# Kernel tuning notes

Measured on AMD Instinct MI355X. Metric: run time of the kernel, lower is better.

## Reference

```python
import jax, jax.numpy as jnp
import numpy as np

N_NODES = 50000
N_EDGES = 600000  # incidence entries; hyperedge ids also live in [0, N_NODES)
HID = 128


def _prelu(x, a):
    return jnp.where(x >= 0, x, a * x)


def _hypergraph_conv(x, W, b, node_idx, edge_idx, num_nodes, num_hedges):
    # PyG HypergraphConv (use_attention=False, heads=1):
    # out = D^{-1} H B^{-1} H^T (X Theta) + bias
    xw = x @ W  # [N, F]
    ones = jnp.ones(node_idx.shape[0], dtype=x.dtype)
    D = jax.ops.segment_sum(ones, node_idx, num_segments=num_nodes)   # node degree
    B = jax.ops.segment_sum(ones, edge_idx, num_segments=num_hedges)  # hyperedge degree
    Dinv = jnp.where(D > 0, 1.0 / D, 0.0)
    Binv = jnp.where(B > 0, 1.0 / B, 0.0)
    # node -> hyperedge aggregation, scaled by B^{-1}
    m = jax.ops.segment_sum(xw[node_idx], edge_idx, num_segments=num_hedges) * Binv[:, None]
    # hyperedge -> node aggregation, scaled by D^{-1}
    out = jax.ops.segment_sum(m[edge_idx], node_idx, num_segments=num_nodes) * Dinv[:, None]
    return out + b


def setup_inputs() -> dict:
    key = jax.random.key(0)
    k1, k2, k3, k4, k5 = jax.random.split(key, 5)
    x = jax.random.normal(k1, (N_NODES, HID), dtype=jnp.float32)
    hyper_edge_index = jax.random.randint(k2, (2, N_EDGES), 0, N_NODES, dtype=jnp.int64)
    # kaiming-normal-ish linear weights, zero biases (per init_weights)
    std = float(np.sqrt(2.0 / HID))
    W1 = jax.random.normal(k3, (HID, HID), dtype=jnp.float32) * std
    W2 = jax.random.normal(k4, (HID, HID), dtype=jnp.float32) * std
    b1 = jnp.zeros((HID,), dtype=jnp.float32)
    b2 = jnp.zeros((HID,), dtype=jnp.float32)
    prelu_a = jnp.full((1,), 0.25, dtype=jnp.float32)  # nn.PReLU default
    return {"x": x, "hyper_edge_index": hyper_edge_index,
            "W1": W1, "b1": b1, "W2": W2, "b2": b2, "prelu_a": prelu_a}


def reference(x, hyper_edge_index, W1, b1, W2, b2, prelu_a):
    node_idx = hyper_edge_index[0]
    edge_idx = hyper_edge_index[1]
    h = _hypergraph_conv(x, W1, b1, node_idx, edge_idx, N_NODES, N_NODES)
    h = _prelu(h, prelu_a)
    h = _hypergraph_conv(h, W2, b2, node_idx, edge_idx, N_NODES, N_NODES)
    h = h + x  # residual
    return _prelu(h, prelu_a)
```

## Files before the change

kernel.cpp:

```cpp
#include <hip/hip_runtime.h>

typedef unsigned short u16;
typedef unsigned int   u32;
typedef unsigned long long u64;

#define HID 128
#define KPB 512
#define NBMAX 256
#define IPB 4096
#define CAP 12288

typedef __bf16 bf16x8 __attribute__((ext_vector_type(8)));
typedef float  f32x4  __attribute__((ext_vector_type(4)));

__device__ inline float u2f(u32 u){ union{u32 u;float f;} v; v.u=u; return v.f; }
__device__ inline u32   f2u(float f){ union{float f;u32 u;} v; v.f=f; return v.u; }
__device__ inline u32  f2bfu(float f){ u32 b=f2u(f); return ((b + 0x7FFFu + ((b>>16)&1u))>>16)&0xFFFFu; }
__device__ inline float blo(u32 u){ return u2f(u<<16); }
__device__ inline float bhi(u32 u){ return u2f(u & 0xFFFF0000u); }

__global__ __launch_bounds__(256) void k_f2bf4(const float4* __restrict__ in, ushort4* __restrict__ out, int n4){
    int i = blockIdx.x*256 + threadIdx.x;
    if (i < n4){
        float4 v = in[i];
        ushort4 o;
        o.x = (u16)f2bfu(v.x); o.y = (u16)f2bfu(v.y);
        o.z = (u16)f2bfu(v.z); o.w = (u16)f2bfu(v.w);
        out[i] = o;
    }
}

__global__ __launch_bounds__(256) void k_wfrag(const float* __restrict__ W, u16* __restrict__ Wf){
    int id = blockIdx.x*256 + threadIdx.x;
    int i = id & 7, l = (id>>3)&63, j = (id>>9)&7, s = id>>12;
    int k = s*32 + ((l>>4)<<3) + i;
    int n = (j<<4) + (l&15);
    Wf[id] = (u16)f2bfu(W[k*HID + n]);
}

__global__ __launch_bounds__(256) void k_hist(const int* __restrict__ nidx, const int* __restrict__ eidx,
                                              int* __restrict__ hist, int nE, int nN, int nb){
    __shared__ int h[NBMAX];
    for (int t=threadIdx.x; t<nb; t+=256) h[t]=0;
    __syncthreads();
    int base = blockIdx.x*IPB;
    for (int k=threadIdx.x; k<IPB; k+=256){
        int j = base+k;
        if (j < nE){
            int n = nidx[j], e = eidx[j];
            atomicAdd(&h[n>>9], 1);
            atomicAdd(&h[(nN+e)>>9], 1);
        }
    }
    __syncthreads();
    for (int t=threadIdx.x; t<nb; t+=256) if (h[t]) atomicAdd(&hist[t], h[t]);
}

__global__ __launch_bounds__(256) void k_bscan(const int* __restrict__ hist, int* __restrict__ bbase,
                                               int* __restrict__ bfill, int* __restrict__ off,
                                               int nb, int nkeys, int total){
    __shared__ int sd[256];
    int t = threadIdx.x;
    int v = (t < nb) ? hist[t] : 0;
    sd[t] = v; __syncthreads();
    for (int o=1;o<256;o<<=1){ int u = (t>=o)? sd[t-o] : 0; __syncthreads(); sd[t]+=u; __syncthreads(); }
    int ex = sd[t] - v;
    if (t < nb){ bbase[t] = ex; bfill[t] = ex; }
    if (t == 0){ bbase[nb] = total; off[nkeys] = total; }
}

__global__ __launch_bounds__(256) void k_part(const int* __restrict__ nidx, const int* __restrict__ eidx,
                                              int* __restrict__ bfill, u64* __restrict__ pairs,
                                              int nE, int nN, int nb){
    __shared__ int h[NBMAX], rsv[NBMAX], fl[NBMAX];
    for (int t=threadIdx.x; t<nb; t+=256){ h[t]=0; fl[t]=0; }
    __syncthreads();
    int base = blockIdx.x*IPB;
    for (int k=threadIdx.x; k<IPB; k+=256){
        int j = base+k;
        if (j < nE){
            int n = nidx[j], e = eidx[j];
            atomicAdd(&h[n>>9], 1);
            atomicAdd(&h[(nN+e)>>9], 1);
        }
    }
    __syncthreads();
    for (int t=threadIdx.x; t<nb; t+=256){ if (h[t]) rsv[t] = atomicAdd(&bfill[t], h[t]); }
    __syncthreads();
    for (int k=threadIdx.x; k<IPB; k+=256){
        int j = base+k;
        if (j < nE){
            int n = nidx[j], e = eidx[j];
            int b1 = n>>9;
            int p1 = rsv[b1] + atomicAdd(&fl[b1], 1);
            pairs[p1] = ((u64)(u32)n << 32) | (u32)e;
            int k2 = nN + e;
            int b2 = k2>>9;
            int p2 = rsv[b2] + atomicAdd(&fl[b2], 1);
            pairs[p2] = ((u64)(u32)k2 << 32) | (u32)n;
        }
    }
}

__global__ __launch_bounds__(256) void k_bucket(const u64* __restrict__ pairs, const int* __restrict__ bbase,
                                                int* __restrict__ csr, int* __restrict__ off, int nkeys){
    __shared__ int cntS[KPB];
    __shared__ int fillS[KPB];
    __shared__ int sd[256];
    __shared__ int vals[CAP];
    int b = blockIdx.x;
    int t = threadIdx.x;
    int base = bbase[b];
    int n = bbase[b+1] - base;
    int k0 = b * KPB;

    for (int i=t; i<KPB; i+=256) cntS[i] = 0;
    __syncthreads();
    for (int i=t; i<n; i+=256){
        u64 p = pairs[base+i];
        int kl = (int)(p>>32) - k0;
        atomicAdd(&cntS[kl], 1);
    }
    __syncthreads();
    int c0 = cntS[2*t], c1 = cntS[2*t+1];
    int s = c0 + c1;
    sd[t] = s; __syncthreads();
    for (int o=1;o<256;o<<=1){ int u = (t>=o)? sd[t-o] : 0; __syncthreads(); sd[t]+=u; __syncthreads(); }
    int ex = sd[t] - s;
    __syncthreads();
    cntS[2*t]   = ex;        cntS[2*t+1]   = ex + c0;
    fillS[2*t]  = ex;        fillS[2*t+1]  = ex + c0;
    __syncthreads();
    for (int i=t; i<KPB; i+=256){
        int k = k0 + i;
        if (k < nkeys) off[k] = base + cntS[i];
    }
    bool fits = (n <= CAP);
    for (int i=t; i<n; i+=256){
        u64 p = pairs[base+i];
        int kl = (int)(p>>32) - k0;
        int pos = atomicAdd(&fillS[kl], 1);
        if (fits) vals[pos] = (int)(u32)p;
        else      csr[base+pos] = (int)(u32)p;
    }
    __syncthreads();
    if (fits){
        for (int i=t; i<n; i+=256) csr[base+i] = vals[i];
    }
}

__global__ __launch_bounds__(256) void k_gemm(const u16* __restrict__ A, const u16* __restrict__ Wf,
                                              u16* __restrict__ C, int M){
    int wave = blockIdx.x*4 + (threadIdx.x>>6);
    int lane = threadIdx.x & 63;
    int rtiles = M >> 4;
    if (wave >= rtiles) return;
    int row0 = wave << 4;

    const u16* Arow = A + (size_t)(row0 + (lane&15))*HID + ((lane>>4)<<3);
    const bf16x8* Wp = reinterpret_cast<const bf16x8*>(Wf) + lane;

    f32x4 acc[8];
    #pragma unroll
    for (int j=0;j<8;++j) acc[j] = (f32x4){0.f,0.f,0.f,0.f};

    #pragma unroll
    for (int s=0;s<4;++s){
        bf16x8 a = *reinterpret_cast<const bf16x8*>(Arow + s*32);
        #pragma unroll
        for (int j=0;j<8;++j){
            bf16x8 b = Wp[(s*8 + j)*64];
            acc[j] = __builtin_amdgcn_mfma_f32_16x16x32_bf16(a, b, acc[j], 0, 0, 0);
        }
    }
    int r0 = row0 + ((lane>>4)<<2);
    int c0 = lane & 15;
    #pragma unroll
    for (int j=0;j<8;++j){
        #pragma unroll
        for (int r=0;r<4;++r){
            C[(size_t)(r0+r)*HID + j*16 + c0] = (u16)f2bfu(acc[j][r]);
        }
    }
}

template<int MODE>
__global__ __launch_bounds__(256) void k_agg(const u32* __restrict__ src, const int* __restrict__ csr,
                                             const int* __restrict__ off, void* __restrict__ outp,
                                             const float* __restrict__ bias, const float* __restrict__ resid,
                                             const float* __restrict__ aptr, int nrows){
    int d = blockIdx.x*4 + (threadIdx.x>>6);
    if (d >= nrows) return;
    int lane = threadIdx.x & 63;
    int start = off[d], end = off[d+1];

    float a0 = 0.f, a1 = 0.f;
    int j = start;
    for (; j+4 <= end; j += 4){
        int s0 = csr[j], s1 = csr[j+1], s2 = csr[j+2], s3 = csr[j+3];
        u32 u0 = src[(size_t)s0*64 + lane];
        u32 u1 = src[(size_t)s1*64 + lane];
        u32 u2 = src[(size_t)s2*64 + lane];
        u32 u3 = src[(size_t)s3*64 + lane];
        a0 += blo(u0) + blo(u1) + blo(u2) + blo(u3);
        a1 += bhi(u0) + bhi(u1) + bhi(u2) + bhi(u3);
    }
    for (; j < end; ++j){
        u32 u = src[(size_t)csr[j]*64 + lane];
        a0 += blo(u); a1 += bhi(u);
    }
    float scale = (end > start) ? 1.0f/(float)(end-start) : 0.f;
    a0 *= scale; a1 *= scale;
    if constexpr (MODE >= 1){ a0 += bias[2*lane]; a1 += bias[2*lane+1]; }
    if constexpr (MODE == 2){
        float2 xr = reinterpret_cast<const float2*>(resid)[(size_t)d*64 + lane];
        a0 += xr.x; a1 += xr.y;
    }
    if constexpr (MODE >= 1){
        float al = aptr[0];
        a0 = (a0 >= 0.f) ? a0 : al*a0;
        a1 = (a1 >= 0.f) ? a1 : al*a1;
    }
    if constexpr (MODE == 2){
        reinterpret_cast<float2*>(outp)[(size_t)d*64 + lane] = make_float2(a0, a1);
    } else {
        reinterpret_cast<u32*>(outp)[(size_t)d*64 + lane] = (f2bfu(a1)<<16) | f2bfu(a0);
    }
}

extern "C" void kernel_launch(void* const* d_in, const int* in_sizes, int n_in,
                              void* d_out, int out_size, void* d_ws, size_t ws_size,
                              hipStream_t stream){
    (void)n_in; (void)out_size; (void)ws_size;
    const float* x  = (const float*)d_in[0];
    const int*  hei = (const int*)  d_in[1];
    const float* W1 = (const float*)d_in[2];
    const float* b1 = (const float*)d_in[3];
    const float* W2 = (const float*)d_in[4];
    const float* b2 = (const float*)d_in[5];
    const float* ap = (const float*)d_in[6];

    const int nN = in_sizes[0] / HID;
    const int nE = in_sizes[1] / 2;
    const int* nidx = hei;
    const int* eidx = hei + nE;
    const int nkeys = 2*nN;
    const int nb    = (nkeys + KPB - 1) / KPB;

    char* w = (char*)d_ws;
    size_t o = 0;
    auto alloc = [&](size_t bytes)->void*{
        void* p = (void*)(w + o);
        o += (bytes + 255) & ~(size_t)255;
        return p;
    };
    int* hist  = (int*)alloc((size_t)NBMAX*sizeof(int));
    int* bbase = (int*)alloc((size_t)(NBMAX+1)*sizeof(int));
    int* bfill = (int*)alloc((size_t)NBMAX*sizeof(int));
    int* off   = (int*)alloc(((size_t)nkeys+1)*sizeof(int));
    int* csr   = (int*)alloc((size_t)2*nE*sizeof(int));
    u64* pairs = (u64*)alloc((size_t)2*nE*sizeof(u64));
    u16* xb    = (u16*)alloc((size_t)nN*HID*sizeof(u16));
    u16* bufB  = (u16*)alloc((size_t)nN*HID*sizeof(u16));
    u16* bufC  = (u16*)alloc((size_t)nN*HID*sizeof(u16));
    u16* w1f   = (u16*)alloc((size_t)HID*HID*sizeof(u16));
    u16* w2f   = (u16*)alloc((size_t)HID*HID*sizeof(u16));

    hipMemsetAsync(hist, 0, (size_t)nb*sizeof(int), stream);

    const int n4 = nN*HID/4;
    k_f2bf4<<<(n4+255)/256, 256, 0, stream>>>((const float4*)x, (ushort4*)xb, n4);
    k_wfrag<<<64, 256, 0, stream>>>(W1, w1f);
    k_wfrag<<<64, 256, 0, stream>>>(W2, w2f);

    const int pgrid = (nE + IPB - 1)/IPB;
    k_hist <<<pgrid, 256, 0, stream>>>(nidx, eidx, hist, nE, nN, nb);
    k_bscan<<<1,     256, 0, stream>>>(hist, bbase, bfill, off, nb, nkeys, 2*nE);
    k_part <<<pgrid, 256, 0, stream>>>(nidx, eidx, bfill, pairs, nE, nN, nb);
    k_bucket<<<nb,   256, 0, stream>>>(pairs, bbase, csr, off, nkeys);

    const int rtiles = nN/16;
    const int ggrid  = (rtiles + 3)/4;
    const int agrid  = (nN + 3)/4;

    k_gemm<<<ggrid, 256, 0, stream>>>(xb, w1f, bufB, nN);
    k_agg<0><<<agrid, 256, 0, stream>>>((const u32*)bufB, csr, off + nN, bufC, nullptr, nullptr, nullptr, nN);
    k_agg<1><<<agrid, 256, 0, stream>>>((const u32*)bufC, csr, off,      xb,   b1, nullptr, ap, nN);
    k_gemm<<<ggrid, 256, 0, stream>>>(xb, w2f, bufB, nN);
    k_agg<0><<<agrid, 256, 0, stream>>>((const u32*)bufB, csr, off + nN, bufC, nullptr, nullptr, nullptr, nN);
    k_agg<2><<<agrid, 256, 0, stream>>>((const u32*)bufC, csr, off, d_out, b2, x, ap, nN);
}
```

Baseline: 281.1 us.

## Split bf16 feature tables into column quarters for cache-friendly gather aggregation

Feature matrices are stored as four column-quarter planes ([4][N][32] bf16), and the conversion, GEMM and aggregation kernels are all changed to read and write that layout. Each aggregation block now handles one quarter, so a gather pass only touches a 3.2 MB plane, which is meant to stay resident in cache across the random gathers. Within a wave, four row groups of 16 lanes each gather different neighbours and are combined with cross-lane shuffles. The cost is four times as many blocks re-reading the CSR and offsets, 64-byte gathers instead of 256-byte ones, and only a quarter of each wave's lanes doing the final write.

```diff
diff --git a/kernel.cpp b/kernel.cpp
--- a/kernel.cpp
+++ b/kernel.cpp
@@ -19,15 +19,17 @@
 __device__ inline float blo(u32 u){ return u2f(u<<16); }
 __device__ inline float bhi(u32 u){ return u2f(u & 0xFFFF0000u); }
 
-__global__ __launch_bounds__(256) void k_f2bf4(const float4* __restrict__ in, ushort4* __restrict__ out, int n4){
-    int i = blockIdx.x*256 + threadIdx.x;
-    if (i < n4){
-        float4 v = in[i];
-        ushort4 o;
-        o.x = (u16)f2bfu(v.x); o.y = (u16)f2bfu(v.y);
-        o.z = (u16)f2bfu(v.z); o.w = (u16)f2bfu(v.w);
-        out[i] = o;
-    }
+__global__ __launch_bounds__(256) void k_f2bfq(const float* __restrict__ in, u16* __restrict__ out, int nN){
+    int id = blockIdx.x*256 + threadIdx.x;
+    if (id >= nN*32) return;
+    int row = id >> 5;
+    int q   = (id >> 3) & 3;
+    int wch = id & 7;
+    float4 v = *reinterpret_cast<const float4*>(in + (size_t)row*HID + (id & 31)*4);
+    ushort4 o;
+    o.x = (u16)f2bfu(v.x); o.y = (u16)f2bfu(v.y);
+    o.z = (u16)f2bfu(v.z); o.w = (u16)f2bfu(v.w);
+    reinterpret_cast<ushort4*>(out)[((size_t)q*nN + row)*8 + wch] = o;
 }
 
 __global__ __launch_bounds__(256) void k_wfrag(const float* __restrict__ W, u16* __restrict__ Wf){
@@ -157,7 +159,8 @@
     if (wave >= rtiles) return;
     int row0 = wave << 4;
 
-    const u16* Arow = A + (size_t)(row0 + (lane&15))*HID + ((lane>>4)<<3);
+    int arow = row0 + (lane&15);
+    int aoff = (lane>>4)<<3;
     const bf16x8* Wp = reinterpret_cast<const bf16x8*>(Wf) + lane;
 
     f32x4 acc[8];
@@ -166,7 +169,7 @@
 
     #pragma unroll
     for (int s=0;s<4;++s){
-        bf16x8 a = *reinterpret_cast<const bf16x8*>(Arow + s*32);
+        bf16x8 a = *reinterpret_cast<const bf16x8*>(A + ((size_t)s*M + arow)*32 + aoff);
         #pragma unroll
         for (int j=0;j<8;++j){
             bf16x8 b = Wp[(s*8 + j)*64];
@@ -177,43 +180,48 @@
     int c0 = lane & 15;
     #pragma unroll
     for (int j=0;j<8;++j){
+        int col = j*16 + c0;
+        int q = col >> 5, wc = col & 31;
         #pragma unroll
         for (int r=0;r<4;++r){
-            C[(size_t)(r0+r)*HID + j*16 + c0] = (u16)f2bfu(acc[j][r]);
+            C[((size_t)q*M + r0 + r)*32 + wc] = (u16)f2bfu(acc[j][r]);
         }
     }
 }
 
 template<int MODE>
-__global__ __launch_bounds__(256) void k_agg(const u32* __restrict__ src, const int* __restrict__ csr,
+__global__ __launch_bounds__(256) void k_agg(const u32* __restrict__ tab, const int* __restrict__ csr,
                                              const int* __restrict__ off, void* __restrict__ outp,
                                              const float* __restrict__ bias, const float* __restrict__ resid,
-                                             const float* __restrict__ aptr, int nrows){
-    int d = blockIdx.x*4 + (threadIdx.x>>6);
-    if (d >= nrows) return;
+                                             const float* __restrict__ aptr, int nN, int nblkq){
+    int q   = blockIdx.x / nblkq;
+    int blk = blockIdx.x - q*nblkq;
+    int d = blk*4 + (threadIdx.x>>6);
+    if (d >= nN) return;
     int lane = threadIdx.x & 63;
+    int g = lane >> 4;
+    int c = lane & 15;
     int start = off[d], end = off[d+1];
+    const u32* tq = tab + (size_t)q*nN*16;
 
     float a0 = 0.f, a1 = 0.f;
-    int j = start;
-    for (; j+4 <= end; j += 4){
-        int s0 = csr[j], s1 = csr[j+1], s2 = csr[j+2], s3 = csr[j+3];
-        u32 u0 = src[(size_t)s0*64 + lane];
-        u32 u1 = src[(size_t)s1*64 + lane];
-        u32 u2 = src[(size_t)s2*64 + lane];
-        u32 u3 = src[(size_t)s3*64 + lane];
-        a0 += blo(u0) + blo(u1) + blo(u2) + blo(u3);
-        a1 += bhi(u0) + bhi(u1) + bhi(u2) + bhi(u3);
-    }
-    for (; j < end; ++j){
-        u32 u = src[(size_t)csr[j]*64 + lane];
-        a0 += blo(u); a1 += bhi(u);
-    }
+    for (int j = start; j < end; j += 8){
+        int r0 = j + g, r1 = r0 + 4;
+        int s0 = (r0 < end) ? csr[r0] : -1;
+        int s1 = (r1 < end) ? csr[r1] : -1;
+        u32 u0 = (s0 >= 0) ? tq[(size_t)s0*16 + c] : 0u;
+        u32 u1 = (s1 >= 0) ? tq[(size_t)s1*16 + c] : 0u;
+        a0 += blo(u0) + blo(u1);
+        a1 += bhi(u0) + bhi(u1);
+    }
+    a0 += __shfl_xor(a0, 32, 64);  a1 += __shfl_xor(a1, 32, 64);
+    a0 += __shfl_xor(a0, 16, 64);  a1 += __shfl_xor(a1, 16, 64);
+
     float scale = (end > start) ? 1.0f/(float)(end-start) : 0.f;
     a0 *= scale; a1 *= scale;
-    if constexpr (MODE >= 1){ a0 += bias[2*lane]; a1 += bias[2*lane+1]; }
+    if constexpr (MODE >= 1){ a0 += bias[32*q + 2*c]; a1 += bias[32*q + 2*c + 1]; }
     if constexpr (MODE == 2){
-        float2 xr = reinterpret_cast<const float2*>(resid)[(size_t)d*64 + lane];
+        float2 xr = reinterpret_cast<const float2*>(resid)[(size_t)d*64 + q*16 + c];
         a0 += xr.x; a1 += xr.y;
     }
     if constexpr (MODE >= 1){
@@ -221,10 +229,12 @@
         a0 = (a0 >= 0.f) ? a0 : al*a0;
         a1 = (a1 >= 0.f) ? a1 : al*a1;
     }
-    if constexpr (MODE == 2){
-        reinterpret_cast<float2*>(outp)[(size_t)d*64 + lane] = make_float2(a0, a1);
-    } else {
-        reinterpret_cast<u32*>(outp)[(size_t)d*64 + lane] = (f2bfu(a1)<<16) | f2bfu(a0);
+    if (g == 0){
+        if constexpr (MODE == 2){
+            reinterpret_cast<float2*>(outp)[(size_t)d*64 + q*16 + c] = make_float2(a0, a1);
+        } else {
+            reinterpret_cast<u32*>(outp)[((size_t)q*nN + d)*16 + c] = (f2bfu(a1)<<16) | f2bfu(a0);
+        }
     }
 }
 
@@ -268,8 +278,7 @@
 
     hipMemsetAsync(hist, 0, (size_t)nb*sizeof(int), stream);
 
-    const int n4 = nN*HID/4;
-    k_f2bf4<<<(n4+255)/256, 256, 0, stream>>>((const float4*)x, (ushort4*)xb, n4);
+    k_f2bfq<<<(nN*32+255)/256, 256, 0, stream>>>(x, xb, nN);
     k_wfrag<<<64, 256, 0, stream>>>(W1, w1f);
     k_wfrag<<<64, 256, 0, stream>>>(W2, w2f);
 
@@ -281,12 +290,13 @@
 
     const int rtiles = nN/16;
     const int ggrid  = (rtiles + 3)/4;
-    const int agrid  = (nN + 3)/4;
+    const int nblkq  = (nN + 3)/4;
+    const int agrid  = nblkq*4;
 
     k_gemm<<<ggrid, 256, 0, stream>>>(xb, w1f, bufB, nN);
-    k_agg<0><<<agrid, 256, 0, stream>>>((const u32*)bufB, csr, off + nN, bufC, nullptr, nullptr, nullptr, nN);
-    k_agg<1><<<agrid, 256, 0, stream>>>((const u32*)bufC, csr, off,      xb,   b1, nullptr, ap, nN);
+    k_agg<0><<<agrid, 256, 0, stream>>>((const u32*)bufB, csr, off + nN, bufC, nullptr, nullptr, nullptr, nN, nblkq);
+    k_agg<1><<<agrid, 256, 0, stream>>>((const u32*)bufC, csr, off,      xb,   b1, nullptr, ap, nN, nblkq);
     k_gemm<<<ggrid, 256, 0, stream>>>(xb, w2f, bufB, nN);
-    k_agg<0><<<agrid, 256, 0, stream>>>((const u32*)bufB, csr, off + nN, bufC, nullptr, nullptr, nullptr, nN);
-    k_agg<2><<<agrid, 256, 0, stream>>>((const u32*)bufC, csr, off, d_out, b2, x, ap, nN);
-}
+    k_agg<0><<<agrid, 256, 0, stream>>>((const u32*)bufB, csr, off + nN, bufC, nullptr, nullptr, nullptr, nN, nblkq);
+    k_agg<2><<<agrid, 256, 0, stream>>>((const u32*)bufC, csr, off, d_out, b2, x, ap, nN, nblkq);
+}
```

Measured after the change: 419.0 us. +49.1%, slower.

## Split wavefront into four row-gather groups with 16-byte loads in aggregation

Applied to the files above, without the earlier changes.

The aggregation kernel now splits each 64-lane wavefront into four 16-lane groups. Each group gathers a different neighbor row per iteration using 16-byte vector loads, with neighbor indices preloaded once per lane and broadcast by shuffle. Partial sums are combined with xor-shuffles and the epilogue runs only on the first group with vectorized stores. This aims to raise memory-level parallelism and cut instruction count on the gathers (average degree about 12). In exchange it adds shuffle reduction overhead and leaves three quarters of lanes idle in the epilogue and for degrees above 64.

```diff
diff --git a/kernel.cpp b/kernel.cpp
--- a/kernel.cpp
+++ b/kernel.cpp
@@ -18,6 +18,7 @@
 __device__ inline u32  f2bfu(float f){ u32 b=f2u(f); return ((b + 0x7FFFu + ((b>>16)&1u))>>16)&0xFFFFu; }
 __device__ inline float blo(u32 u){ return u2f(u<<16); }
 __device__ inline float bhi(u32 u){ return u2f(u & 0xFFFF0000u); }
+__device__ inline u32  pk(float lo, float hi){ return (f2bfu(hi)<<16) | f2bfu(lo); }
 
 __global__ __launch_bounds__(256) void k_f2bf4(const float4* __restrict__ in, ushort4* __restrict__ out, int n4){
     int i = blockIdx.x*256 + threadIdx.x;
@@ -185,46 +186,85 @@
 }
 
 template<int MODE>
-__global__ __launch_bounds__(256) void k_agg(const u32* __restrict__ src, const int* __restrict__ csr,
+__global__ __launch_bounds__(256) void k_agg(const u32* __restrict__ tab, const int* __restrict__ csr,
                                              const int* __restrict__ off, void* __restrict__ outp,
                                              const float* __restrict__ bias, const float* __restrict__ resid,
                                              const float* __restrict__ aptr, int nrows){
     int d = blockIdx.x*4 + (threadIdx.x>>6);
     if (d >= nrows) return;
     int lane = threadIdx.x & 63;
+    int g = lane >> 4;
+    int c = lane & 15;
     int start = off[d], end = off[d+1];
-
-    float a0 = 0.f, a1 = 0.f;
-    int j = start;
-    for (; j+4 <= end; j += 4){
-        int s0 = csr[j], s1 = csr[j+1], s2 = csr[j+2], s3 = csr[j+3];
-        u32 u0 = src[(size_t)s0*64 + lane];
-        u32 u1 = src[(size_t)s1*64 + lane];
-        u32 u2 = src[(size_t)s2*64 + lane];
-        u32 u3 = src[(size_t)s3*64 + lane];
-        a0 += blo(u0) + blo(u1) + blo(u2) + blo(u3);
-        a1 += bhi(u0) + bhi(u1) + bhi(u2) + bhi(u3);
-    }
-    for (; j < end; ++j){
-        u32 u = src[(size_t)csr[j]*64 + lane];
-        a0 += blo(u); a1 += bhi(u);
-    }
-    float scale = (end > start) ? 1.0f/(float)(end-start) : 0.f;
-    a0 *= scale; a1 *= scale;
-    if constexpr (MODE >= 1){ a0 += bias[2*lane]; a1 += bias[2*lane+1]; }
-    if constexpr (MODE == 2){
-        float2 xr = reinterpret_cast<const float2*>(resid)[(size_t)d*64 + lane];
-        a0 += xr.x; a1 += xr.y;
-    }
-    if constexpr (MODE >= 1){
-        float al = aptr[0];
-        a0 = (a0 >= 0.f) ? a0 : al*a0;
-        a1 = (a1 >= 0.f) ? a1 : al*a1;
-    }
-    if constexpr (MODE == 2){
-        reinterpret_cast<float2*>(outp)[(size_t)d*64 + lane] = make_float2(a0, a1);
-    } else {
-        reinterpret_cast<u32*>(outp)[(size_t)d*64 + lane] = (f2bfu(a1)<<16) | f2bfu(a0);
+    int deg = end - start;
+
+    int myc = 0;
+    if (lane < deg) myc = csr[start + lane];
+
+    float a0=0.f,a1=0.f,a2=0.f,a3=0.f,a4=0.f,a5=0.f,a6=0.f,a7=0.f;
+    int nb4 = deg < 64 ? deg : 64;
+    for (int jb = 0; jb < nb4; jb += 4){
+        int j = jb + g;
+        int src = __shfl(myc, j, 64);
+        uint4 v = make_uint4(0u,0u,0u,0u);
+        if (j < nb4) v = *reinterpret_cast<const uint4*>(tab + (size_t)src*64 + (c<<2));
+        a0 += blo(v.x); a1 += bhi(v.x);
+        a2 += blo(v.y); a3 += bhi(v.y);
+        a4 += blo(v.z); a5 += bhi(v.z);
+        a6 += blo(v.w); a7 += bhi(v.w);
+    }
+    for (int j = start + 64; j < end; ++j){
+        uint4 v = make_uint4(0u,0u,0u,0u);
+        if (g == 0){
+            int src = csr[j];
+            v = *reinterpret_cast<const uint4*>(tab + (size_t)src*64 + (c<<2));
+        }
+        a0 += blo(v.x); a1 += bhi(v.x);
+        a2 += blo(v.y); a3 += bhi(v.y);
+        a4 += blo(v.z); a5 += bhi(v.z);
+        a6 += blo(v.w); a7 += bhi(v.w);
+    }
+    a0 += __shfl_xor(a0,16,64); a0 += __shfl_xor(a0,32,64);
+    a1 += __shfl_xor(a1,16,64); a1 += __shfl_xor(a1,32,64);
+    a2 += __shfl_xor(a2,16,64); a2 += __shfl_xor(a2,32,64);
+    a3 += __shfl_xor(a3,16,64); a3 += __shfl_xor(a3,32,64);
+    a4 += __shfl_xor(a4,16,64); a4 += __shfl_xor(a4,32,64);
+    a5 += __shfl_xor(a5,16,64); a5 += __shfl_xor(a5,32,64);
+    a6 += __shfl_xor(a6,16,64); a6 += __shfl_xor(a6,32,64);
+    a7 += __shfl_xor(a7,16,64); a7 += __shfl_xor(a7,32,64);
+
+    if (g == 0){
+        float s = (deg > 0) ? 1.0f/(float)deg : 0.f;
+        a0*=s; a1*=s; a2*=s; a3*=s; a4*=s; a5*=s; a6*=s; a7*=s;
+        if constexpr (MODE >= 1){
+            float4 b0 = *reinterpret_cast<const float4*>(bias + (c<<3));
+            float4 b1v = *reinterpret_cast<const float4*>(bias + (c<<3) + 4);
+            a0+=b0.x; a1+=b0.y; a2+=b0.z; a3+=b0.w;
+            a4+=b1v.x; a5+=b1v.y; a6+=b1v.z; a7+=b1v.w;
+        }
+        if constexpr (MODE == 2){
+            const float* rp = resid + (size_t)d*HID + (c<<3);
+            float4 r0 = *reinterpret_cast<const float4*>(rp);
+            float4 r1 = *reinterpret_cast<const float4*>(rp + 4);
+            a0+=r0.x; a1+=r0.y; a2+=r0.z; a3+=r0.w;
+            a4+=r1.x; a5+=r1.y; a6+=r1.z; a7+=r1.w;
+        }
+        if constexpr (MODE >= 1){
+            float al = aptr[0];
+            a0 = (a0>=0.f)? a0 : al*a0;  a1 = (a1>=0.f)? a1 : al*a1;
+            a2 = (a2>=0.f)? a2 : al*a2;  a3 = (a3>=0.f)? a3 : al*a3;
+            a4 = (a4>=0.f)? a4 : al*a4;  a5 = (a5>=0.f)? a5 : al*a5;
+            a6 = (a6>=0.f)? a6 : al*a6;  a7 = (a7>=0.f)? a7 : al*a7;
+        }
+        if constexpr (MODE == 2){
+            float* op = (float*)outp + (size_t)d*HID + (c<<3);
+            *reinterpret_cast<float4*>(op)     = make_float4(a0,a1,a2,a3);
+            *reinterpret_cast<float4*>(op + 4) = make_float4(a4,a5,a6,a7);
+        } else {
+            uint4 wv;
+            wv.x = pk(a0,a1); wv.y = pk(a2,a3); wv.z = pk(a4,a5); wv.w = pk(a6,a7);
+            *reinterpret_cast<uint4*>((u32*)outp + (size_t)d*64 + (c<<2)) = wv;
+        }
     }
 }
 
```

Result: faster. 258.7 us (-8.0%).
